# Kernel optimization log

Hardware: AMD Instinct MI355X
Metric: run time of the kernel (lower is better)

## Reference

```python
import jax, jax.numpy as jnp
import numpy as np

# Module constants (from init_kwargs)
MAP_BBOX = (-5.0, -5.0, 5.0, 5.0)  # h1, w1, h2, w2
V_BBOX = (0.0, 3.0)
MAP_RES = (64, 64)
V_RES = 8
XYZ_TO_H, XYZ_TO_W, XYZ_TO_V = 0, 1, 2
SCALE = 4
PCN_H = 64


def mish(x):
    return x * jnp.tanh(jax.nn.softplus(x))


def conv_d2(x, w):
    # 3x3 conv, dilation 2, padding 2, stride 1, no bias (NCHW / OIHW)
    return jax.lax.conv_general_dilated(
        x, w, window_strides=(1, 1), padding=((2, 2), (2, 2)),
        rhs_dilation=(2, 2), dimension_numbers=('NCHW', 'OIHW', 'NCHW'))


def maxpool3s2(x):
    # MaxPool2d(kernel=3, stride=2, padding=1); torch pads with -inf
    return jax.lax.reduce_window(
        x, -jnp.inf, jax.lax.max,
        window_dimensions=(1, 1, 3, 3), window_strides=(1, 1, 2, 2),
        padding=((0, 0), (0, 0), (1, 1), (1, 1)))


def setup_inputs() -> dict:
    key = jax.random.key(0)
    k1, k2, k3, k4, k5 = jax.random.split(key, 5)
    N, H, W = 64, 256, 256
    B = 8
    return {
        'rgb': jax.random.normal(k1, (N, 3, H, W), dtype=jnp.float32),
        'surf_xyz': jax.random.normal(k2, (N, 3, H, W), dtype=jnp.float32),
        'W1': jax.random.normal(k3, (PCN_H, 3, 3, 3), dtype=jnp.float32) * 0.1,
        'W2': jax.random.normal(k4, (PCN_H, PCN_H, 3, 3), dtype=jnp.float32) * 0.05,
        'index': jax.random.randint(k5, (N,), 0, B, dtype=jnp.int32),
        'batch_size': B,
    }


def reference(rgb, surf_xyz, W1, W2, index, batch_size):
    N, _, H, W = surf_xyz.shape
    s = SCALE
    Hs, Ws = H // s, W // s

    # avg_pool2d(rgb, 4)
    surf_rgb = rgb.reshape(N, 3, Hs, s, Ws, s).mean(axis=(3, 5))
    # subsampled xyz: surf_xyz[:, :, 2::4, 2::4]
    sxyz = surf_xyz[:, :, s // 2::s, s // 2::s]  # (N,3,Hs,Ws)
    _index = jnp.broadcast_to(index[:, None, None], (N, Hs, Ws))

    # rgb_conv_net: conv -> mish -> maxpool -> conv -> mish -> maxpool (dropout=0)
    feat = maxpool3s2(mish(conv_d2(rgb, W1)))
    feat = maxpool3s2(mish(conv_d2(feat, W2)))  # (N, h, Hs, Ws)

    # flatten  (valid_points is None path)
    hdim = feat.shape[1]
    flat_features = feat.transpose(0, 2, 3, 1).reshape(-1, hdim)   # (M, h)
    flat_xyz = sxyz.transpose(0, 2, 3, 1).reshape(-1, 3)           # (M, 3)
    flat_rgb = surf_rgb.transpose(0, 2, 3, 1).reshape(-1, 3)       # (M, 3)
    flat_index = _index.reshape(-1)                                # (M,)

    # coord_to_grid (float->int cast truncates toward zero, matching torch .long())
    map_h, map_w = MAP_RES
    h1, w1, h2, w2 = MAP_BBOX
    v1, v2 = V_BBOX
    hs = ((flat_xyz[:, XYZ_TO_H] - h1) * map_h / (h2 - h1)).astype(jnp.int32)
    ws = ((flat_xyz[:, XYZ_TO_W] - w1) * map_w / (w2 - w1)).astype(jnp.int32)
    vs = ((flat_xyz[:, XYZ_TO_V] - v1) * V_RES / (v2 - v1)).astype(jnp.int32)
    valid = ((hs >= 0) & (hs < map_h) & (ws >= 0) & (ws < map_w)
             & (vs >= 0) & (vs < V_RES))

    B, V = batch_size, V_RES
    P = B * V * map_h * map_w
    lin = ((flat_index * V + vs) * map_h + hs) * map_w + ws
    # route invalid points to a dummy segment that gets dropped
    lin_safe = jnp.where(valid, lin, P)

    sums = jax.ops.segment_sum(flat_features, lin_safe, num_segments=P + 1)[:P]
    rgbs = jax.ops.segment_sum(flat_rgb, lin_safe, num_segments=P + 1)[:P]
    counts = jax.ops.segment_sum(
        jnp.ones_like(lin_safe), lin_safe, num_segments=P + 1)[:P]

    feature_map = sums.reshape(B, V, map_h, map_w, hdim).transpose(0, 4, 1, 2, 3)
    rgb_map = rgbs.reshape(B, V, map_h, map_w, 3).transpose(0, 4, 1, 2, 3)
    feature_counts = counts.reshape(B, V, map_h, map_w)[:, None]
    return feature_map, feature_counts, rgb_map
```

## Files before the change

kernel.cpp:

```cpp
#include <hip/hip_runtime.h>
#include <hip/hip_bf16.h>
#include <math.h>

#define N_IMG 64
#define CH    64
#define F1_R  136
#define F1_C  136
#define F1_IMG_STRIDE ((size_t)F1_R * F1_C * 64)
#define F1_ROW_STRIDE (F1_C * 64)
#define FEAT1_BYTES ((size_t)N_IMG * F1_IMG_STRIDE * 2)
#define LINPT_BYTES (262144 * 4)

#define OUT_CNT_BASE 16777216
#define OUT_RGB_BASE 17039360

typedef short bf16x8 __attribute__((ext_vector_type(8)));
typedef float f32x4  __attribute__((ext_vector_type(4)));

__device__ __forceinline__ float fast_mish(float x) {
    float xc = fminf(x, 20.0f);
    float t  = __expf(xc);
    float n  = t * (t + 2.0f);
    float y  = x * n / (n + 2.0f);
    return (x > 20.0f) ? x : y;
}

__device__ __forceinline__ unsigned short f2bf(float f) {
    unsigned u = __float_as_uint(f);
    unsigned r = (u + 0x7FFFu + ((u >> 16) & 1u)) >> 16;
    return (unsigned short)r;
}

__global__ __launch_bounds__(256) void w2cvt_kernel(
    const float* __restrict__ w2, unsigned short* __restrict__ w2bf)
{
    int i = blockIdx.x * 256 + threadIdx.x;
    if (i < 36864) {
        int t  = i >> 12;
        int co = (i >> 6) & 63;
        int ci = i & 63;
        w2bf[i] = f2bf(w2[(co * 64 + ci) * 9 + t]);
    }
}

__global__ __launch_bounds__(256) void point_kernel(
    const float* __restrict__ rgb,
    const float* __restrict__ sxyz,
    const int*   __restrict__ index,
    float*       __restrict__ out,
    int*         __restrict__ lin_pt)
{
    int p = blockIdx.x * 256 + threadIdx.x;
    int n  = p >> 12;
    int r  = p & 4095;
    int hs = r >> 6;
    int ws = r & 63;

    int row = hs * 4 + 2, col = ws * 4 + 2;
    const float* sx = sxyz + (size_t)n * 3 * 65536;
    float X = sx[row * 256 + col];
    float Y = sx[65536 + row * 256 + col];
    float Z = sx[2 * 65536 + row * 256 + col];

    int hb = (int)(((X + 5.0f) * 64.0f) / 10.0f);
    int wb = (int)(((Y + 5.0f) * 64.0f) / 10.0f);
    int vb = (int)((Z * 8.0f) / 3.0f);
    bool valid = (hb >= 0) & (hb < 64) & (wb >= 0) & (wb < 64) & (vb >= 0) & (vb < 8);

    int b   = index[n];
    int lin = ((b * 8 + vb) * 64 + hb) * 64 + wb;
    lin_pt[p] = valid ? lin : -1;

    if (valid) {
        atomicAdd(out + OUT_CNT_BASE + lin, 1.0f);
        int rem = lin & 32767;
        #pragma unroll
        for (int c = 0; c < 3; c++) {
            const float* rg = rgb + (size_t)(n * 3 + c) * 65536;
            float s = 0.0f;
            #pragma unroll
            for (int i = 0; i < 4; i++)
                #pragma unroll
                for (int j = 0; j < 4; j++)
                    s += rg[(hs * 4 + i) * 256 + (ws * 4 + j)];
            atomicAdd(out + OUT_RGB_BASE + b * 98304 + c * 32768 + rem, s * 0.0625f);
        }
    }
}

__global__ __launch_bounds__(1024) void conv1_mfma_kernel(
    const float* __restrict__ rgb,
    const float* __restrict__ w1,
    __hip_bfloat16* __restrict__ feat1)
{
    int b2 = ((blockIdx.x & 7) << 9) + (blockIdx.x >> 3);
    const int n  = b2 >> 6;
    const int pr = b2 & 63;
    const int tid  = threadIdx.x;
    const int lane = tid & 63;
    const int w    = tid >> 6;

    __shared__ __align__(16) char smem[81920];
    unsigned short* wlds = (unsigned short*)smem;
    unsigned short* in_t = (unsigned short*)(smem + 4096);

    for (int i = tid; i < 2048; i += 1024) {
        int co = i >> 5, k = i & 31;
        wlds[i] = (k < 27) ? f2bf(w1[co * 27 + k]) : (unsigned short)0;
    }
    {
        const float* img = rgb + (size_t)n * 3 * 65536;
        for (int i = tid; i < 7144; i += 1024) {
            unsigned short v = 0;
            if (i < 7128) {
                int ci  = i / 2376;
                int rem = i - ci * 2376;
                int rr  = rem / 264;
                int cc  = rem - rr * 264;
                int gy  = 4 * pr - 3 + rr;
                int gx  = cc - 2;
                if (gy >= 0 && gy < 256 && gx >= 0 && gx < 256)
                    v = f2bf(img[ci * 65536 + gy * 256 + gx]);
            }
            in_t[i] = v;
        }
    }
    __syncthreads();

    int boff[8];
    #pragma unroll
    for (int j = 0; j < 8; j++) {
        int k = ((lane >> 4) << 3) + j;
        if (k < 27) {
            int ci = k / 9, t = k - 9 * ci, ky = t / 3, kx = t - 3 * ky;
            boff[j] = (ci * 2376 + 2 * ky * 264 + 2 * kx + (lane & 15)) * 2;
        } else {
            boff[j] = 7128 * 2;
        }
    }

    bf16x8 a[4];
    #pragma unroll
    for (int mt = 0; mt < 4; mt++)
        a[mt] = *reinterpret_cast<const bf16x8*>(
            wlds + (mt * 16 + (lane & 15)) * 32 + ((lane >> 4) << 3));

    f32x4 acc[5][4];
    #pragma unroll
    for (int tt = 0; tt < 5; tt++)
        #pragma unroll
        for (int mt = 0; mt < 4; mt++)
            acc[tt][mt] = (f32x4){0.f, 0.f, 0.f, 0.f};

    const char* in_b = (const char*)in_t;
    #pragma unroll
    for (int tt = 0; tt < 5; tt++) {
        int t5 = w * 5 + tt;
        int r  = t5 >> 4;
        int x0 = (t5 & 15) << 4;
        int base = (r * 264 + x0) * 2;
        unsigned short e[8];
        #pragma unroll
        for (int j = 0; j < 8; j++)
            e[j] = *reinterpret_cast<const unsigned short*>(in_b + base + boff[j]);
        bf16x8 b;
        #pragma unroll
        for (int j = 0; j < 8; j++) b[j] = (short)e[j];
        #pragma unroll
        for (int mt = 0; mt < 4; mt++)
            acc[tt][mt] = __builtin_amdgcn_mfma_f32_16x16x32_bf16(a[mt], b, acc[tt][mt], 0, 0, 0);
    }

    __syncthreads();

    unsigned short* pool = (unsigned short*)smem;
    const int ybase = 4 * pr - 1;

    #pragma unroll
    for (int p = 0; p < 2; p++) {
        #pragma unroll
        for (int tt = 0; tt < 5; tt++) {
            int t5 = w * 5 + tt;
            int r  = t5 >> 4;
            int x  = ((t5 & 15) << 4) + (lane & 15);
            bool dead = (ybase + r) < 0;
            #pragma unroll
            for (int m2 = 0; m2 < 2; m2++) {
                int mt  = p * 2 + m2;
                int col = m2 * 16 + ((lane >> 4) << 2);
                unsigned long long pk = 0;
                #pragma unroll
                for (int q = 0; q < 4; q++) {
                    float v = dead ? -INFINITY : fast_mish(acc[tt][mt][q]);
                    pk |= (unsigned long long)f2bf(v) << (16 * q);
                }
                int byte = (((r * 256 + x) * 32) + col) * 2;
                byte ^= (x & 7) << 4;
                *reinterpret_cast<unsigned long long*>((char*)pool + byte) = pk;
            }
        }
        __syncthreads();
        for (int i = tid; i < 8192; i += 1024) {
            int pp = i >> 12;
            int c  = (i >> 5) & 127;
            int cl = i & 31;
            float m = -INFINITY;
            #pragma unroll
            for (int dy = 0; dy < 3; dy++) {
                int lr = 2 * pp + dy;
                #pragma unroll
                for (int dx = 0; dx < 3; dx++) {
                    int x = 2 * c - 1 + dx;
                    if (x < 0) continue;
                    int byte = ((((lr * 256) + x) * 32) + cl) * 2;
                    byte ^= (x & 7) << 4;
                    unsigned short hv = *reinterpret_cast<const unsigned short*>((char*)pool + byte);
                    m = fmaxf(m, __uint_as_float((unsigned)hv << 16));
                }
            }
            unsigned short* dst = (unsigned short*)(feat1 + (size_t)n * F1_IMG_STRIDE
                + (size_t)(2 * pr + pp + 4) * F1_ROW_STRIDE + (size_t)(c + 4) * 64 + p * 32 + cl);
            *dst = f2bf(m);
        }
        __syncthreads();
    }
}

__global__ __launch_bounds__(640) void conv2_mfma_kernel(
    const __hip_bfloat16* __restrict__ feat1,
    const unsigned short* __restrict__ w2bf,
    const int*   __restrict__ lin_pt,
    float*       __restrict__ out)
{
    int b2 = ((blockIdx.x & 7) << 8) + (blockIdx.x >> 3);
    const int n  = b2 >> 5;
    const int pr = b2 & 31;
    const int tid  = threadIdx.x;
    const int lane = tid & 63;
    const int w    = tid >> 6;
    const int lrow = w >> 1;
    const int chalf = w & 1;
    const int y = 4 * pr - 1 + lrow;

    __shared__ __align__(16) char smem[40960];

    f32x4 acc[4][4];
    #pragma unroll
    for (int mt = 0; mt < 4; mt++)
        #pragma unroll
        for (int nt = 0; nt < 4; nt++)
            acc[mt][nt] = (f32x4){0.f, 0.f, 0.f, 0.f};

    const __hip_bfloat16* bbase = feat1 + (size_t)n * F1_IMG_STRIDE
        + ((size_t)(y + 2) * F1_C + (lane & 15) + chalf * 64 + 2) * 64
        + ((lane >> 4) << 3);
    const unsigned short* abase = w2bf + (size_t)(lane & 15) * 64 + ((lane >> 4) << 3);

    #pragma unroll
    for (int ky = 0; ky < 3; ky++) {
        #pragma unroll
        for (int kx = 0; kx < 3; kx++) {
            const int t = ky * 3 + kx;
            #pragma unroll
            for (int s = 0; s < 2; s++) {
                bf16x8 a[4];
                #pragma unroll
                for (int mt = 0; mt < 4; mt++)
                    a[mt] = *reinterpret_cast<const bf16x8*>(
                        abase + ((t * 64 + mt * 16) * 64) + s * 32);
                const __hip_bfloat16* bp = bbase + (ky * 2 * F1_C + kx * 2) * 64 + s * 32;
                #pragma unroll
                for (int nt = 0; nt < 4; nt++) {
                    bf16x8 b = *reinterpret_cast<const bf16x8*>(bp + nt * 1024);
                    #pragma unroll
                    for (int mt = 0; mt < 4; mt++)
                        acc[mt][nt] = __builtin_amdgcn_mfma_f32_16x16x32_bf16(
                            a[mt], b, acc[mt][nt], 0, 0, 0);
                }
            }
        }
    }

    const bool deadrow = (y < 0);
    const int pbase = (n << 12) + ((pr << 1) << 6);

    #pragma unroll
    for (int p = 0; p < 2; p++) {
        if (p) __syncthreads();
        #pragma unroll
        for (int nt = 0; nt < 4; nt++) {
            int col = chalf * 64 + nt * 16 + (lane & 15);
            #pragma unroll
            for (int m2 = 0; m2 < 2; m2++) {
                int mt  = p * 2 + m2;
                int cl0 = m2 * 16 + ((lane >> 4) << 2);
                unsigned long long pk = 0;
                #pragma unroll
                for (int r4 = 0; r4 < 4; r4++) {
                    float v = deadrow ? -INFINITY : fast_mish(acc[mt][nt][r4]);
                    pk |= (unsigned long long)f2bf(v) << (16 * r4);
                }
                int byte = (((lrow * 128 + col) * 32) + cl0) * 2;
                byte ^= (col & 7) << 4;
                *reinterpret_cast<unsigned long long*>(smem + byte) = pk;
            }
        }
        __syncthreads();
        for (int i = tid; i < 4096; i += 640) {
            int pp = i >> 11;
            int c  = (i >> 5) & 63;
            int cl = i & 31;
            float m = -INFINITY;
            #pragma unroll
            for (int dy = 0; dy < 3; dy++) {
                int lr = 2 * pp + dy;
                #pragma unroll
                for (int dx = 0; dx < 3; dx++) {
                    int x = 2 * c - 1 + dx;
                    if (x < 0 || x > 127) continue;
                    int byte = ((((lr * 128 + x) * 32) + cl) * 2) ^ ((x & 7) << 4);
                    unsigned short hv = *reinterpret_cast<const unsigned short*>(smem + byte);
                    m = fmaxf(m, __uint_as_float((unsigned)hv << 16));
                }
            }
            int lin = lin_pt[pbase + (pp << 6) + c];
            if (lin >= 0)
                atomicAdd(out + (size_t)(lin >> 15) * 2097152
                              + (size_t)(p * 32 + cl) * 32768 + (lin & 32767), m);
        }
    }
}

extern "C" void kernel_launch(void* const* d_in, const int* in_sizes, int n_in,
                              void* d_out, int out_size, void* d_ws, size_t ws_size,
                              hipStream_t stream)
{
    const float* rgb   = (const float*)d_in[0];
    const float* sxyz  = (const float*)d_in[1];
    const float* w1    = (const float*)d_in[2];
    const float* w2    = (const float*)d_in[3];
    const int*   index = (const int*)d_in[4];
    float* out = (float*)d_out;

    __hip_bfloat16* feat1 = (__hip_bfloat16*)d_ws;
    int* lin_pt = (int*)((char*)d_ws + FEAT1_BYTES);
    unsigned short* w2bf = (unsigned short*)((char*)d_ws + FEAT1_BYTES + LINPT_BYTES);

    hipMemsetAsync(d_out, 0, (size_t)out_size * 4, stream);
    hipMemsetAsync(d_ws, 0, FEAT1_BYTES, stream);

    w2cvt_kernel<<<144, 256, 0, stream>>>(w2, w2bf);
    point_kernel<<<1024, 256, 0, stream>>>(rgb, sxyz, index, out, lin_pt);
    conv1_mfma_kernel<<<4096, 1024, 0, stream>>>(rgb, w1, feat1);
    conv2_mfma_kernel<<<2048, 640, 0, stream>>>(feat1, w2bf, lin_pt, out);
}
```

Baseline: 1.287 ms.

## Split conv2 output channels across two blocks and stage weights in LDS

Each conv2 block now computes only 32 of the 64 output channels, which doubles the grid to 4096 blocks and halves the accumulators per thread. The block's half of the bf16 weights is copied into swizzled shared memory up front, so A fragments are read from LDS instead of global memory. The launch bounds also ask for more waves per CU. In exchange, every input-feature B fragment is now loaded by two blocks instead of one, and each block pays for an extra weight-staging pass and barrier.

```diff
diff --git a/kernel.cpp b/kernel.cpp
--- a/kernel.cpp
+++ b/kernel.cpp
@@ -226,15 +226,16 @@
     }
 }
 
-__global__ __launch_bounds__(640) void conv2_mfma_kernel(
+__global__ __launch_bounds__(640, 5) void conv2_mfma_kernel(
     const __hip_bfloat16* __restrict__ feat1,
     const unsigned short* __restrict__ w2bf,
     const int*   __restrict__ lin_pt,
     float*       __restrict__ out)
 {
-    int b2 = ((blockIdx.x & 7) << 8) + (blockIdx.x >> 3);
-    const int n  = b2 >> 5;
-    const int pr = b2 & 31;
+    int b2 = ((blockIdx.x & 7) << 9) + (blockIdx.x >> 3);
+    const int n   = b2 >> 6;
+    const int pr  = (b2 >> 1) & 31;
+    const int ch2 = b2 & 1;
     const int tid  = threadIdx.x;
     const int lane = tid & 63;
     const int w    = tid >> 6;
@@ -244,9 +245,19 @@
 
     __shared__ __align__(16) char smem[40960];
 
-    f32x4 acc[4][4];
-    #pragma unroll
-    for (int mt = 0; mt < 4; mt++)
+    for (int i = tid; i < 18432; i += 640) {
+        int t    = i >> 11;
+        int co32 = (i >> 6) & 31;
+        int ci   = i & 63;
+        int byte = (((((t << 5) + co32) << 6) + ci) << 1) ^ ((co32 & 7) << 4);
+        *reinterpret_cast<unsigned short*>(smem + byte) =
+            w2bf[((t << 6) + ch2 * 32 + co32) * 64 + ci];
+    }
+    __syncthreads();
+
+    f32x4 acc[2][4];
+    #pragma unroll
+    for (int mt = 0; mt < 2; mt++)
         #pragma unroll
         for (int nt = 0; nt < 4; nt++)
             acc[mt][nt] = (f32x4){0.f, 0.f, 0.f, 0.f};
@@ -254,7 +265,6 @@
     const __hip_bfloat16* bbase = feat1 + (size_t)n * F1_IMG_STRIDE
         + ((size_t)(y + 2) * F1_C + (lane & 15) + chalf * 64 + 2) * 64
         + ((lane >> 4) << 3);
-    const unsigned short* abase = w2bf + (size_t)(lane & 15) * 64 + ((lane >> 4) << 3);
 
     #pragma unroll
     for (int ky = 0; ky < 3; ky++) {
@@ -263,17 +273,20 @@
             const int t = ky * 3 + kx;
             #pragma unroll
             for (int s = 0; s < 2; s++) {
-                bf16x8 a[4];
-                #pragma unroll
-                for (int mt = 0; mt < 4; mt++)
-                    a[mt] = *reinterpret_cast<const bf16x8*>(
-                        abase + ((t * 64 + mt * 16) * 64) + s * 32);
+                bf16x8 a[2];
+                #pragma unroll
+                for (int mt = 0; mt < 2; mt++) {
+                    int co32 = mt * 16 + (lane & 15);
+                    int abyte = (((((t << 5) + co32) << 6) + (s << 5) + ((lane >> 4) << 3)) << 1)
+                                ^ ((co32 & 7) << 4);
+                    a[mt] = *reinterpret_cast<const bf16x8*>(smem + abyte);
+                }
                 const __hip_bfloat16* bp = bbase + (ky * 2 * F1_C + kx * 2) * 64 + s * 32;
                 #pragma unroll
                 for (int nt = 0; nt < 4; nt++) {
                     bf16x8 b = *reinterpret_cast<const bf16x8*>(bp + nt * 1024);
                     #pragma unroll
-                    for (int mt = 0; mt < 4; mt++)
+                    for (int mt = 0; mt < 2; mt++)
                         acc[mt][nt] = __builtin_amdgcn_mfma_f32_16x16x32_bf16(
                             a[mt], b, acc[mt][nt], 0, 0, 0);
                 }
@@ -281,53 +294,49 @@
         }
     }
 
+    __syncthreads();
+
     const bool deadrow = (y < 0);
+    #pragma unroll
+    for (int nt = 0; nt < 4; nt++) {
+        int col = chalf * 64 + nt * 16 + (lane & 15);
+        #pragma unroll
+        for (int mt = 0; mt < 2; mt++) {
+            int cl0 = mt * 16 + ((lane >> 4) << 2);
+            unsigned long long pk = 0;
+            #pragma unroll
+            for (int r4 = 0; r4 < 4; r4++) {
+                float v = deadrow ? -INFINITY : fast_mish(acc[mt][nt][r4]);
+                pk |= (unsigned long long)f2bf(v) << (16 * r4);
+            }
+            int byte = ((((lrow * 128 + col) * 32) + cl0) * 2) ^ ((col & 7) << 4);
+            *reinterpret_cast<unsigned long long*>(smem + byte) = pk;
+        }
+    }
+    __syncthreads();
+
     const int pbase = (n << 12) + ((pr << 1) << 6);
-
-    #pragma unroll
-    for (int p = 0; p < 2; p++) {
-        if (p) __syncthreads();
-        #pragma unroll
-        for (int nt = 0; nt < 4; nt++) {
-            int col = chalf * 64 + nt * 16 + (lane & 15);
-            #pragma unroll
-            for (int m2 = 0; m2 < 2; m2++) {
-                int mt  = p * 2 + m2;
-                int cl0 = m2 * 16 + ((lane >> 4) << 2);
-                unsigned long long pk = 0;
-                #pragma unroll
-                for (int r4 = 0; r4 < 4; r4++) {
-                    float v = deadrow ? -INFINITY : fast_mish(acc[mt][nt][r4]);
-                    pk |= (unsigned long long)f2bf(v) << (16 * r4);
-                }
-                int byte = (((lrow * 128 + col) * 32) + cl0) * 2;
-                byte ^= (col & 7) << 4;
-                *reinterpret_cast<unsigned long long*>(smem + byte) = pk;
-            }
-        }
-        __syncthreads();
-        for (int i = tid; i < 4096; i += 640) {
-            int pp = i >> 11;
-            int c  = (i >> 5) & 63;
-            int cl = i & 31;
-            float m = -INFINITY;
-            #pragma unroll
-            for (int dy = 0; dy < 3; dy++) {
-                int lr = 2 * pp + dy;
-                #pragma unroll
-                for (int dx = 0; dx < 3; dx++) {
-                    int x = 2 * c - 1 + dx;
-                    if (x < 0 || x > 127) continue;
-                    int byte = ((((lr * 128 + x) * 32) + cl) * 2) ^ ((x & 7) << 4);
-                    unsigned short hv = *reinterpret_cast<const unsigned short*>(smem + byte);
-                    m = fmaxf(m, __uint_as_float((unsigned)hv << 16));
-                }
-            }
-            int lin = lin_pt[pbase + (pp << 6) + c];
-            if (lin >= 0)
-                atomicAdd(out + (size_t)(lin >> 15) * 2097152
-                              + (size_t)(p * 32 + cl) * 32768 + (lin & 32767), m);
-        }
+    for (int i = tid; i < 4096; i += 640) {
+        int pp = i >> 11;
+        int c  = (i >> 5) & 63;
+        int cl = i & 31;
+        float m = -INFINITY;
+        #pragma unroll
+        for (int dy = 0; dy < 3; dy++) {
+            int lr = 2 * pp + dy;
+            #pragma unroll
+            for (int dx = 0; dx < 3; dx++) {
+                int x = 2 * c - 1 + dx;
+                if (x < 0 || x > 127) continue;
+                int byte = ((((lr * 128 + x) * 32) + cl) * 2) ^ ((x & 7) << 4);
+                unsigned short hv = *reinterpret_cast<const unsigned short*>(smem + byte);
+                m = fmaxf(m, __uint_as_float((unsigned)hv << 16));
+            }
+        }
+        int lin = lin_pt[pbase + (pp << 6) + c];
+        if (lin >= 0)
+            atomicAdd(out + (size_t)(lin >> 15) * 2097152
+                          + (size_t)(ch2 * 32 + cl) * 32768 + (lin & 32767), m);
     }
 }
 
@@ -352,5 +361,5 @@
     w2cvt_kernel<<<144, 256, 0, stream>>>(w2, w2bf);
     point_kernel<<<1024, 256, 0, stream>>>(rgb, sxyz, index, out, lin_pt);
     conv1_mfma_kernel<<<4096, 1024, 0, stream>>>(rgb, w1, feat1);
-    conv2_mfma_kernel<<<2048, 640, 0, stream>>>(feat1, w2bf, lin_pt, out);
-}
+    conv2_mfma_kernel<<<4096, 640, 0, stream>>>(feat1, w2bf, lin_pt, out);
+}
```

Result: faster. 1.241 ms (-3.6%).
